# Optimization experiments

Measured on AMD Instinct MI355X. Metric: run time of the kernel, lower is better.

The kernel has to match this reference:

```python
import jax, jax.numpy as jnp
import numpy as np

N = 100000
E = 1600000
F_IN = 512
S_IN = 6
H = 64
C = 7


def gcn_conv(x, W, b, row, col, n):
    # PyG GCNConv: linear (no bias in lin), add self-loops, sym-normalize, scatter-add, + bias
    x = x @ W  # [N, out]
    loop = jnp.arange(n)
    r = jnp.concatenate([row, loop])
    c = jnp.concatenate([col, loop])
    deg = jax.ops.segment_sum(jnp.ones(r.shape, x.dtype), c, num_segments=n)
    dinv = jnp.where(deg > 0, deg ** -0.5, 0.0)
    norm = dinv[r] * dinv[c]  # [E+N]
    out = jax.ops.segment_sum(x[r] * norm[:, None], c, num_segments=n)
    return out + b


def setup_inputs() -> dict:
    key = jax.random.key(0)
    ks = jax.random.split(key, 12)
    feature = jax.random.normal(ks[0], (N, F_IN), jnp.float32)
    structure = jax.random.normal(ks[1], (N, S_IN), jnp.float32)
    edge_index = jax.random.randint(ks[2], (2, E), 0, N, dtype=jnp.int64)
    # glorot-ish param init
    def w(k, fan_in, fan_out):
        return jax.random.normal(k, (fan_in, fan_out), jnp.float32) * (1.0 / np.sqrt(fan_in))
    return {
        "feature": feature,
        "structure": structure,
        "edge_index": edge_index,
        "W_f": w(ks[3], F_IN, H), "b_f": jnp.zeros((H,), jnp.float32),
        "W_s": w(ks[4], S_IN, H), "b_s": jnp.zeros((H,), jnp.float32),
        "W_r": w(ks[5], 2 * H, C), "b_r": jnp.zeros((C,), jnp.float32),
        "emb": jax.random.normal(ks[6], (6, H), jnp.float32),
        "embW": jax.random.normal(ks[7], (H, 1), jnp.float32),
        "alpha_s": jnp.asarray(0.4, jnp.float32),
        "alpha_a": jnp.asarray(0.6, jnp.float32),
    }


def reference(feature, structure, edge_index, W_f, b_f, W_s, b_s, W_r, b_r, emb, embW, alpha_s, alpha_a):
    row, col = edge_index[0], edge_index[1]
    # branch 1: feature GCN (dropout is identity in eval mode)
    h_f = gcn_conv(feature, W_f, b_f, row, col, N)
    attr = h_f
    # embedding gate: sigmoid(emb @ embW) thresholded at 0.5 -> {0,1}
    gate = jax.nn.sigmoid(emb @ embW)  # [6,1]
    gate = jnp.where(gate < 0.5, 0.0, 1.0).astype(feature.dtype)
    struct_in = structure * gate[:, 0][None, :]  # [N,6] * [1,6]
    # branch 2: structure GCN
    h_s = gcn_conv(struct_in, W_s, b_s, row, col, N)
    struc = h_s
    # L1-normalize alphas (0.4,0.6 already sum to 1; torch does it via .data)
    denom = jax.lax.stop_gradient(jnp.abs(alpha_s) + jnp.abs(alpha_a))
    a_s = alpha_s / denom
    a_a = alpha_a / denom
    x = jnp.concatenate([attr * a_a * 2.0, struc * a_s * 2.0], axis=1)  # [N, 2H]
    y = gcn_conv(x, W_r, b_r, row, col, N)
    return (h_f, h_s, y)
```

## Files before the change

kernel.cpp:

```cpp
#include <hip/hip_runtime.h>
#include <hip/hip_bf16.h>


typedef __attribute__((ext_vector_type(8))) short bf16x8;
typedef __attribute__((ext_vector_type(4))) float f32x4;

__device__ __forceinline__ unsigned short f2bf(float x) {
    union { __hip_bfloat16 b; unsigned short u; } cv;
    cv.b = __float2bfloat16(x);
    return cv.u;
}
__device__ __forceinline__ float bf2f(unsigned short u) {
    union { unsigned u32; float f; } cv;
    cv.u32 = ((unsigned)u) << 16;
    return cv.f;
}

__device__ __forceinline__ void gload16(const void* g, void* l) {
    __builtin_amdgcn_global_load_lds(
        (const __attribute__((address_space(1))) void*)g,
        (__attribute__((address_space(3))) void*)l, 16, 0, 0);
}

__global__ __launch_bounds__(256) void setup_prep_k(const float* __restrict__ emb,
                                                    const float* __restrict__ embW,
                                                    const float* __restrict__ alpha_s,
                                                    const float* __restrict__ alpha_a,
                                                    float* __restrict__ cw,
                                                    const float* __restrict__ Wf,
                                                    unsigned short* __restrict__ WthG,
                                                    unsigned short* __restrict__ WtlG,
                                                    unsigned* __restrict__ deg, int n) {
    if (blockIdx.x == 0) {
        if (threadIdx.x >= 64) return;
        int lane = threadIdx.x;
        float w = embW[lane];
        #pragma unroll
        for (int k = 0; k < 6; k++) {
            float p = emb[k * 64 + lane] * w;
            #pragma unroll
            for (int off = 32; off; off >>= 1) p += __shfl_xor(p, off);
            if (lane == 0) cw[k] = (p < 0.0f) ? 0.0f : 1.0f;
        }
        if (lane == 0) {
            float s = alpha_s[0];
            float a = alpha_a[0];
            float inv = 1.0f / (fabsf(s) + fabsf(a));
            cw[6] = 2.0f * a * inv;
            cw[7] = 2.0f * s * inv;
        }
        return;
    }
    if (blockIdx.x <= 128) {
        int idx = (blockIdx.x - 1) * 256 + threadIdx.x;
        int k = idx >> 6, c = idx & 63;
        float w = Wf[idx];
        unsigned short h = f2bf(w);
        unsigned short l = f2bf(w - bf2f(h));
        WthG[c * 512 + k] = h;
        WtlG[c * 512 + k] = l;
        return;
    }
    int start = (blockIdx.x - 129) * 1024 + threadIdx.x;
    #pragma unroll
    for (int k = 0; k < 4; k++) {
        int w = start + k * 256;
        if (w < n) deg[w] = 0u;
    }
}

__device__ __forceinline__ bool detect32(const int* p32, int e, int E, int lane) {
    int se = (e < E) ? e : lane;
    return __any(p32[2 * se + 1] != 0);
}

#define CHUNK 4096
__global__ __launch_bounds__(256) void degfill_k(const void* __restrict__ ei,
                                                 unsigned* __restrict__ deg,
                                                 int* __restrict__ slot, int E, int n) {
    int range = blockIdx.x & 7;
    int nper = (n + 7) >> 3;
    int lo = range * nper;
    int hi = min(n, lo + nper);
    int e0 = (blockIdx.x >> 3) * CHUNK + threadIdx.x;
    int lane = threadIdx.x & 63;
    const int* p32 = (const int*)ei;
    bool is32 = detect32(p32, e0, E, lane);

    int cs[16];
    #pragma unroll
    for (int k = 0; k < 16; k++) {
        int e = e0 + k * 256;
        cs[k] = -1;
        if (e < E)
            cs[k] = is32 ? p32[E + e] : (int)((const long long*)ei)[(size_t)E + e];
    }
    #pragma unroll
    for (int k = 0; k < 16; k++) {
        int c = cs[k];
        if (c < lo || c >= hi) continue;
        int e = e0 + k * 256;
        int r = is32 ? p32[e] : (int)((const long long*)ei)[(size_t)e];
        unsigned pos = atomicAdd(&deg[c], 1u);
        if (pos < 64u) slot[((size_t)c << 6) + pos] = r;
    }
}

__global__ void dinv_ss6_k(const unsigned* __restrict__ deg, float* __restrict__ dinv,
                           const float* __restrict__ structure, const float* __restrict__ cw,
                           unsigned short* __restrict__ ss6, int n) {
    int i = blockIdx.x * 256 + threadIdx.x;
    if (i >= n) return;
    float dv = rsqrtf((float)deg[i] + 1.0f);
    dinv[i] = dv;
    #pragma unroll
    for (int k = 0; k < 6; k++) ss6[i * 8 + k] = f2bf(structure[i * 6 + k] * cw[k] * dv);
    ss6[i * 8 + 6] = 0;
    ss6[i * 8 + 7] = 0;
}

__global__ __launch_bounds__(256) void gemm_f_mfma(const float* __restrict__ feat,
                                                   const unsigned short* __restrict__ WthG,
                                                   const unsigned short* __restrict__ WtlG,
                                                   const float* __restrict__ dinv,
                                                   unsigned short* __restrict__ xs, int n) {
    __shared__ float          Afp[64 * 64];
    __shared__ unsigned short Bh[64 * 64];
    __shared__ unsigned short Bl[64 * 64];

    const int tid = threadIdx.x;
    const int w = tid >> 6, l = tid & 63;
    const int lr = l & 15, lg = l >> 4;
    const int rowbase = blockIdx.x * 64;

    f32x4 acc[4];
    #pragma unroll
    for (int nt = 0; nt < 4; nt++) acc[nt] = (f32x4)(0.0f);

    const int arow = w * 16 + lr;
    const int asw = (arow & 7) << 4;
    const char* Ab = (const char*)Afp + arow * 256;

    for (int c = 0; c < 8; c++) {
        #pragma unroll
        for (int j = 0; j < 4; j++) {
            int inst = j * 4 + w;
            int g = inst * 64 + l;
            int r = g >> 4;
            int kbs = ((g & 15) << 4) ^ ((r & 7) << 4);
            const float* src = feat + (size_t)min(rowbase + r, n - 1) * 512 + c * 64 + (kbs >> 2);
            gload16(src, (char*)Afp + inst * 1024);
        }
        #pragma unroll
        for (int j = 0; j < 2; j++) {
            int inst = j * 4 + w;
            int g = inst * 64 + l;
            int col = g >> 3;
            int kbs = ((g & 7) << 4) ^ ((col & 7) << 4);
            gload16(WthG + (size_t)col * 512 + c * 64 + (kbs >> 1), (char*)Bh + inst * 1024);
            gload16(WtlG + (size_t)col * 512 + c * 64 + (kbs >> 1), (char*)Bl + inst * 1024);
        }
        __syncthreads();
        #pragma unroll
        for (int ks = 0; ks < 2; ks++) {
            int kb0 = ks * 128 + lg * 32;
            float4 f0 = *(const float4*)(Ab + (kb0 ^ asw));
            float4 f1 = *(const float4*)(Ab + ((kb0 + 16) ^ asw));
            bf16x8 a;
            a[0] = (short)f2bf(f0.x); a[1] = (short)f2bf(f0.y);
            a[2] = (short)f2bf(f0.z); a[3] = (short)f2bf(f0.w);
            a[4] = (short)f2bf(f1.x); a[5] = (short)f2bf(f1.y);
            a[6] = (short)f2bf(f1.z); a[7] = (short)f2bf(f1.w);
            int kb = ks * 64 + lg * 16;
            #pragma unroll
            for (int nt = 0; nt < 4; nt++) {
                int bc = nt * 16 + lr;
                int cb = bc * 128 + (kb ^ ((bc & 7) << 4));
                bf16x8 bh = *(const bf16x8*)((const char*)Bh + cb);
                bf16x8 bl = *(const bf16x8*)((const char*)Bl + cb);
                acc[nt] = __builtin_amdgcn_mfma_f32_16x16x32_bf16(a, bh, acc[nt], 0, 0, 0);
                acc[nt] = __builtin_amdgcn_mfma_f32_16x16x32_bf16(a, bl, acc[nt], 0, 0, 0);
            }
        }
        __syncthreads();
    }
    int row0 = rowbase + w * 16 + lg * 4;
    #pragma unroll
    for (int reg = 0; reg < 4; reg++) {
        int gr = row0 + reg;
        if (gr < n) {
            float dv = dinv[gr];
            #pragma unroll
            for (int nt = 0; nt < 4; nt++)
                xs[(size_t)gr * 64 + nt * 16 + lr] = f2bf(acc[nt][reg] * dv);
        }
    }
}

#define GATHER8(rl, g, accv, a6v)                                              \
    {                                                                          \
        int r0 = __shfl(rl, g + 0), r1 = __shfl(rl, g + 1);                    \
        int r2 = __shfl(rl, g + 2), r3 = __shfl(rl, g + 3);                    \
        int r4 = __shfl(rl, g + 4), r5 = __shfl(rl, g + 5);                    \
        int r6 = __shfl(rl, g + 6), r7 = __shfl(rl, g + 7);                    \
        float v0 = bf2f(xs[(size_t)r0 * 64 + lane]);                           \
        float v1 = bf2f(xs[(size_t)r1 * 64 + lane]);                           \
        float v2 = bf2f(xs[(size_t)r2 * 64 + lane]);                           \
        float v3 = bf2f(xs[(size_t)r3 * 64 + lane]);                           \
        float v4 = bf2f(xs[(size_t)r4 * 64 + lane]);                           \
        float v5 = bf2f(xs[(size_t)r5 * 64 + lane]);                           \
        float v6 = bf2f(xs[(size_t)r6 * 64 + lane]);                           \
        float v7 = bf2f(xs[(size_t)r7 * 64 + lane]);                           \
        accv += ((v0 + v1) + (v2 + v3)) + ((v4 + v5) + (v6 + v7));             \
        if (lane < 6) {                                                        \
            float u0 = bf2f(ss6[r0 * 8 + lane]), u1 = bf2f(ss6[r1 * 8 + lane]);\
            float u2 = bf2f(ss6[r2 * 8 + lane]), u3 = bf2f(ss6[r3 * 8 + lane]);\
            float u4 = bf2f(ss6[r4 * 8 + lane]), u5 = bf2f(ss6[r5 * 8 + lane]);\
            float u6 = bf2f(ss6[r6 * 8 + lane]), u7 = bf2f(ss6[r7 * 8 + lane]);\
            a6v += ((u0 + u1) + (u2 + u3)) + ((u4 + u5) + (u6 + u7));          \
        }                                                                      \
    }

__global__ __launch_bounds__(256) void agg_fs_k(const unsigned short* __restrict__ xs,
                                                const unsigned short* __restrict__ ss6,
                                                const int* __restrict__ slot,
                                                const unsigned* __restrict__ deg,
                                                const float* __restrict__ dinv,
                                                const float* __restrict__ cw,
                                                const float* __restrict__ bfv,
                                                const float* __restrict__ Ws,
                                                const float* __restrict__ bs,
                                                const float* __restrict__ Wr,
                                                float* __restrict__ out_hf,
                                                float* __restrict__ out_hs,
                                                unsigned short* __restrict__ ps, int n) {
    int wid = threadIdx.x >> 6;
    int lane = threadIdx.x & 63;
    int iA = blockIdx.x * 8 + wid * 2;
    int iB = iA + 1;
    if (iA >= n) return;
    bool hasB = iB < n;

    int dA = (int)min(deg[iA], 64u);
    int dB = hasB ? (int)min(deg[iB], 64u) : 0;

    float accA = bf2f(xs[(size_t)iA * 64 + lane]);
    float accB = hasB ? bf2f(xs[(size_t)iB * 64 + lane]) : 0.0f;
    float a6A = (lane < 6) ? bf2f(ss6[iA * 8 + lane]) : 0.0f;
    float a6B = (hasB && lane < 6) ? bf2f(ss6[iB * 8 + lane]) : 0.0f;

    int rlA = (lane < dA) ? slot[((size_t)iA << 6) + lane] : 0;
    int rlB = (lane < dB) ? slot[((size_t)iB << 6) + lane] : 0;
    int gmax = max(dA, dB);
    for (int g = 0; g + 8 <= gmax; g += 8) {
        if (g + 8 <= dA) GATHER8(rlA, g, accA, a6A);
        if (g + 8 <= dB) GATHER8(rlB, g, accB, a6B);
    }
    for (int d = dA & ~7; d < dA; d++) {
        int r = __shfl(rlA, d);
        accA += bf2f(xs[(size_t)r * 64 + lane]);
        if (lane < 6) a6A += bf2f(ss6[r * 8 + lane]);
    }
    for (int d = dB & ~7; d < dB; d++) {
        int r = __shfl(rlB, d);
        accB += bf2f(xs[(size_t)r * 64 + lane]);
        if (lane < 6) a6B += bf2f(ss6[r * 8 + lane]);
    }

    #pragma unroll
    for (int node = 0; node < 2; node++) {
        if (node == 1 && !hasB) break;
        int i = node ? iB : iA;
        float acc = node ? accB : accA;
        float a6 = node ? a6B : a6A;
        float di = dinv[i];
        float hf = acc * di + bfv[lane];
        float hs = bs[lane];
        #pragma unroll
        for (int k = 0; k < 6; k++) hs += __shfl(a6, k) * di * Ws[k * 64 + lane];
        out_hf[(size_t)i * 64 + lane] = hf;
        out_hs[(size_t)i * 64 + lane] = hs;

        float fa = hf * cw[6];
        float sa = hs * cw[7];
        #pragma unroll
        for (int j = 0; j < 7; j++) {
            float v = fa * Wr[lane * 7 + j] + sa * Wr[(64 + lane) * 7 + j];
            #pragma unroll
            for (int off = 32; off; off >>= 1) v += __shfl_xor(v, off);
            if (lane == j) ps[(size_t)i * 8 + j] = f2bf(v * di);
        }
        if (lane == 7) ps[(size_t)i * 8 + 7] = 0;
    }
}

__global__ __launch_bounds__(256) void agg_y_k(const unsigned short* __restrict__ ps,
                                               const int* __restrict__ slot,
                                               const unsigned* __restrict__ deg,
                                               const float* __restrict__ dinv,
                                               const float* __restrict__ br,
                                               float* __restrict__ out_y, int n) {
    int i = blockIdx.x * 4 + (threadIdx.x >> 6);
    int lane = threadIdx.x & 63;
    if (i >= n) return;
    int es = lane >> 3, j = lane & 7;
    int cnt = (int)min(deg[i], 64u);
    const int* srow = slot + ((size_t)i << 6);
    float acc = (es == 0) ? bf2f(ps[(size_t)i * 8 + j]) : 0.0f;
    int base = 0;
    for (; base + 16 <= cnt; base += 16) {
        int ra = srow[base + es];
        int rb = srow[base + 8 + es];
        acc += bf2f(ps[(size_t)ra * 8 + j]) + bf2f(ps[(size_t)rb * 8 + j]);
    }
    for (; base < cnt; base += 8) {
        int idx = base + es;
        if (idx < cnt) acc += bf2f(ps[(size_t)srow[idx] * 8 + j]);
    }
    acc += __shfl_xor(acc, 8);
    acc += __shfl_xor(acc, 16);
    acc += __shfl_xor(acc, 32);
    if (j < 7) out_y[(size_t)i * 7 + j] = acc * dinv[i] + br[j];
}

extern "C" void kernel_launch(void* const* d_in, const int* in_sizes, int n_in,
                              void* d_out, int out_size, void* d_ws, size_t ws_size,
                              hipStream_t stream) {
    const float* feature   = (const float*)d_in[0];
    const float* structure = (const float*)d_in[1];
    const void*  ei        = d_in[2];
    const float* Wf  = (const float*)d_in[3];
    const float* bfv = (const float*)d_in[4];
    const float* Ws  = (const float*)d_in[5];
    const float* bs  = (const float*)d_in[6];
    const float* Wr  = (const float*)d_in[7];
    const float* br  = (const float*)d_in[8];
    const float* emb = (const float*)d_in[9];
    const float* embW = (const float*)d_in[10];
    const float* alpha_s = (const float*)d_in[11];
    const float* alpha_a = (const float*)d_in[12];

    const int N = in_sizes[0] / 512;
    const int E = in_sizes[2] / 2;
    const int NB = (N + 255) / 256;
    const int NZ = (N + 1023) / 1024;
    const int NCH = (E + CHUNK - 1) / CHUNK;

    float* ws = (float*)d_ws;
    size_t XS     = 0;
    size_t SS6    = XS + (size_t)N * 32;
    size_t PS     = SS6 + (size_t)N * 4;
    size_t DINV   = PS + (size_t)N * 4;
    size_t DEG    = DINV + N;
    size_t CW     = DEG + N;
    size_t WT     = CW + 16;
    size_t SLOT   = WT + 32768;

    unsigned short* xs = (unsigned short*)(ws + XS);
    unsigned short* ss6 = (unsigned short*)(ws + SS6);
    unsigned short* ps = (unsigned short*)(ws + PS);
    float* dinv = ws + DINV;
    unsigned* deg = (unsigned*)(ws + DEG);
    float* cw = ws + CW;
    unsigned short* WthG = (unsigned short*)(ws + WT);
    unsigned short* WtlG = WthG + 512 * 64;
    int* slot = (int*)(ws + SLOT);

    setup_prep_k<<<129 + NZ, 256, 0, stream>>>(emb, embW, alpha_s, alpha_a, cw,
                                               Wf, WthG, WtlG, deg, N);
    degfill_k<<<NCH * 8, 256, 0, stream>>>(ei, deg, slot, E, N);
    dinv_ss6_k<<<NB, 256, 0, stream>>>(deg, dinv, structure, cw, ss6, N);
    gemm_f_mfma<<<(N + 63) / 64, 256, 0, stream>>>(feature, WthG, WtlG, dinv, xs, N);

    float* out_hf = (float*)d_out;
    float* out_hs = out_hf + (size_t)N * 64;
    float* out_y  = out_hf + (size_t)N * 128;
    agg_fs_k<<<(N + 7) / 8, 256, 0, stream>>>(xs, ss6, slot, deg, dinv, cw,
                                              bfv, Ws, bs, Wr, out_hf, out_hs, ps, N);
    agg_y_k<<<(N + 3) / 4, 256, 0, stream>>>(ps, slot, deg, dinv, br, out_y, N);
}
```

Measured before the change: 264.9 us.

## Fuse degree fill with feature GEMM and apply source normalization in aggregation

Merges the edge bucketing/degree-count kernel and the feature GEMM into one launch with interleaved block roles, so the atomic-heavy scatter and the MFMA GEMM run concurrently instead of back to back. This removes the dependence of the GEMM on dinv: xs and ss6 are stored unnormalized, and the per-source dinv is recomputed from deg inside the gather loops. The dinv_ss6 kernel and dinv buffer are dropped, with the structure gating folded into the setup kernel. In exchange, each gathered neighbour costs an extra deg load and rsqrt, and the mixed block roles may share compute units less evenly.

Result: no change. 264.2 us (-0.2%).

```diff
diff --git a/kernel.cpp b/kernel.cpp
--- a/kernel.cpp
+++ b/kernel.cpp
@@ -30,7 +30,9 @@
                                                     const float* __restrict__ Wf,
                                                     unsigned short* __restrict__ WthG,
                                                     unsigned short* __restrict__ WtlG,
-                                                    unsigned* __restrict__ deg, int n) {
+                                                    unsigned* __restrict__ deg,
+                                                    const float* __restrict__ structure,
+                                                    unsigned short* __restrict__ ss6, int n) {
     if (blockIdx.x == 0) {
         if (threadIdx.x >= 64) return;
         int lane = threadIdx.x;
@@ -61,11 +63,28 @@
         WtlG[c * 512 + k] = l;
         return;
     }
+    int lane = threadIdx.x & 63;
+    float wv = embW[lane];
+    float g[6];
+    #pragma unroll
+    for (int k = 0; k < 6; k++) {
+        float p = emb[k * 64 + lane] * wv;
+        #pragma unroll
+        for (int off = 32; off; off >>= 1) p += __shfl_xor(p, off);
+        g[k] = (p < 0.0f) ? 0.0f : 1.0f;
+    }
     int start = (blockIdx.x - 129) * 1024 + threadIdx.x;
     #pragma unroll
-    for (int k = 0; k < 4; k++) {
-        int w = start + k * 256;
-        if (w < n) deg[w] = 0u;
+    for (int j = 0; j < 4; j++) {
+        int i = start + j * 256;
+        if (i < n) {
+            deg[i] = 0u;
+            #pragma unroll
+            for (int k = 0; k < 6; k++)
+                ss6[i * 8 + k] = f2bf(structure[i * 6 + k] * g[k]);
+            ss6[i * 8 + 6] = 0;
+            ss6[i * 8 + 7] = 0;
+        }
     }
 }
 
@@ -75,63 +94,58 @@
 }
 
 #define CHUNK 4096
-__global__ __launch_bounds__(256) void degfill_k(const void* __restrict__ ei,
-                                                 unsigned* __restrict__ deg,
-                                                 int* __restrict__ slot, int E, int n) {
-    int range = blockIdx.x & 7;
-    int nper = (n + 7) >> 3;
-    int lo = range * nper;
-    int hi = min(n, lo + nper);
-    int e0 = (blockIdx.x >> 3) * CHUNK + threadIdx.x;
-    int lane = threadIdx.x & 63;
-    const int* p32 = (const int*)ei;
-    bool is32 = detect32(p32, e0, E, lane);
-
-    int cs[16];
-    #pragma unroll
-    for (int k = 0; k < 16; k++) {
-        int e = e0 + k * 256;
-        cs[k] = -1;
-        if (e < E)
-            cs[k] = is32 ? p32[E + e] : (int)((const long long*)ei)[(size_t)E + e];
-    }
-    #pragma unroll
-    for (int k = 0; k < 16; k++) {
-        int c = cs[k];
-        if (c < lo || c >= hi) continue;
-        int e = e0 + k * 256;
-        int r = is32 ? p32[e] : (int)((const long long*)ei)[(size_t)e];
-        unsigned pos = atomicAdd(&deg[c], 1u);
-        if (pos < 64u) slot[((size_t)c << 6) + pos] = r;
-    }
-}
-
-__global__ void dinv_ss6_k(const unsigned* __restrict__ deg, float* __restrict__ dinv,
-                           const float* __restrict__ structure, const float* __restrict__ cw,
-                           unsigned short* __restrict__ ss6, int n) {
-    int i = blockIdx.x * 256 + threadIdx.x;
-    if (i >= n) return;
-    float dv = rsqrtf((float)deg[i] + 1.0f);
-    dinv[i] = dv;
-    #pragma unroll
-    for (int k = 0; k < 6; k++) ss6[i * 8 + k] = f2bf(structure[i * 6 + k] * cw[k] * dv);
-    ss6[i * 8 + 6] = 0;
-    ss6[i * 8 + 7] = 0;
-}
-
-__global__ __launch_bounds__(256) void gemm_f_mfma(const float* __restrict__ feat,
-                                                   const unsigned short* __restrict__ WthG,
-                                                   const unsigned short* __restrict__ WtlG,
-                                                   const float* __restrict__ dinv,
-                                                   unsigned short* __restrict__ xs, int n) {
+
+__global__ __launch_bounds__(256) void fused_k(const void* __restrict__ ei,
+                                               unsigned* __restrict__ deg,
+                                               int* __restrict__ slot, int E, int n,
+                                               int GB,
+                                               const float* __restrict__ feat,
+                                               const unsigned short* __restrict__ WthG,
+                                               const unsigned short* __restrict__ WtlG,
+                                               unsigned short* __restrict__ xs) {
     __shared__ float          Afp[64 * 64];
     __shared__ unsigned short Bh[64 * 64];
     __shared__ unsigned short Bl[64 * 64];
 
+    const int b = blockIdx.x;
     const int tid = threadIdx.x;
+    const bool is_gemm = (b % 3 == 2) && (b / 3 < GB);
+
+    if (!is_gemm) {
+        int eb = b - min(GB, b / 3);
+        int range = eb & 7;
+        int nper = (n + 7) >> 3;
+        int lo = range * nper;
+        int hi = min(n, lo + nper);
+        int e0 = (eb >> 3) * CHUNK + tid;
+        int lane = tid & 63;
+        const int* p32 = (const int*)ei;
+        bool is32 = detect32(p32, e0, E, lane);
+
+        int cs[16];
+        #pragma unroll
+        for (int k = 0; k < 16; k++) {
+            int e = e0 + k * 256;
+            cs[k] = -1;
+            if (e < E)
+                cs[k] = is32 ? p32[E + e] : (int)((const long long*)ei)[(size_t)E + e];
+        }
+        #pragma unroll
+        for (int k = 0; k < 16; k++) {
+            int c = cs[k];
+            if (c < lo || c >= hi) continue;
+            int e = e0 + k * 256;
+            int r = is32 ? p32[e] : (int)((const long long*)ei)[(size_t)e];
+            unsigned pos = atomicAdd(&deg[c], 1u);
+            if (pos < 64u) slot[((size_t)c << 6) + pos] = r;
+        }
+        return;
+    }
+
+    const int gb = b / 3;
     const int w = tid >> 6, l = tid & 63;
     const int lr = l & 15, lg = l >> 4;
-    const int rowbase = blockIdx.x * 64;
+    const int rowbase = gb * 64;
 
     f32x4 acc[4];
     #pragma unroll
@@ -189,13 +203,14 @@
     for (int reg = 0; reg < 4; reg++) {
         int gr = row0 + reg;
         if (gr < n) {
-            float dv = dinv[gr];
             #pragma unroll
             for (int nt = 0; nt < 4; nt++)
-                xs[(size_t)gr * 64 + nt * 16 + lr] = f2bf(acc[nt][reg] * dv);
-        }
-    }
-}
+                xs[(size_t)gr * 64 + nt * 16 + lr] = f2bf(acc[nt][reg]);
+        }
+    }
+}
+
+__device__ __forceinline__ float dnv(unsigned d) { return rsqrtf((float)d + 1.0f); }
 
 #define GATHER8(rl, g, accv, a6v)                                              \
     {                                                                          \
@@ -203,20 +218,28 @@
         int r2 = __shfl(rl, g + 2), r3 = __shfl(rl, g + 3);                    \
         int r4 = __shfl(rl, g + 4), r5 = __shfl(rl, g + 5);                    \
         int r6 = __shfl(rl, g + 6), r7 = __shfl(rl, g + 7);                    \
-        float v0 = bf2f(xs[(size_t)r0 * 64 + lane]);                           \
-        float v1 = bf2f(xs[(size_t)r1 * 64 + lane]);                           \
-        float v2 = bf2f(xs[(size_t)r2 * 64 + lane]);                           \
-        float v3 = bf2f(xs[(size_t)r3 * 64 + lane]);                           \
-        float v4 = bf2f(xs[(size_t)r4 * 64 + lane]);                           \
-        float v5 = bf2f(xs[(size_t)r5 * 64 + lane]);                           \
-        float v6 = bf2f(xs[(size_t)r6 * 64 + lane]);                           \
-        float v7 = bf2f(xs[(size_t)r7 * 64 + lane]);                           \
+        float q0 = dnv(deg[r0]), q1 = dnv(deg[r1]);                            \
+        float q2 = dnv(deg[r2]), q3 = dnv(deg[r3]);                            \
+        float q4 = dnv(deg[r4]), q5 = dnv(deg[r5]);                            \
+        float q6 = dnv(deg[r6]), q7 = dnv(deg[r7]);                            \
+        float v0 = bf2f(xs[(size_t)r0 * 64 + lane]) * q0;                      \
+        float v1 = bf2f(xs[(size_t)r1 * 64 + lane]) * q1;                      \
+        float v2 = bf2f(xs[(size_t)r2 * 64 + lane]) * q2;                      \
+        float v3 = bf2f(xs[(size_t)r3 * 64 + lane]) * q3;                      \
+        float v4 = bf2f(xs[(size_t)r4 * 64 + lane]) * q4;                      \
+        float v5 = bf2f(xs[(size_t)r5 * 64 + lane]) * q5;                      \
+        float v6 = bf2f(xs[(size_t)r6 * 64 + lane]) * q6;                      \
+        float v7 = bf2f(xs[(size_t)r7 * 64 + lane]) * q7;                      \
         accv += ((v0 + v1) + (v2 + v3)) + ((v4 + v5) + (v6 + v7));             \
         if (lane < 6) {                                                        \
-            float u0 = bf2f(ss6[r0 * 8 + lane]), u1 = bf2f(ss6[r1 * 8 + lane]);\
-            float u2 = bf2f(ss6[r2 * 8 + lane]), u3 = bf2f(ss6[r3 * 8 + lane]);\
-            float u4 = bf2f(ss6[r4 * 8 + lane]), u5 = bf2f(ss6[r5 * 8 + lane]);\
-            float u6 = bf2f(ss6[r6 * 8 + lane]), u7 = bf2f(ss6[r7 * 8 + lane]);\
+            float u0 = bf2f(ss6[r0 * 8 + lane]) * q0;                          \
+            float u1 = bf2f(ss6[r1 * 8 + lane]) * q1;                          \
+            float u2 = bf2f(ss6[r2 * 8 + lane]) * q2;                          \
+            float u3 = bf2f(ss6[r3 * 8 + lane]) * q3;                          \
+            float u4 = bf2f(ss6[r4 * 8 + lane]) * q4;                          \
+            float u5 = bf2f(ss6[r5 * 8 + lane]) * q5;                          \
+            float u6 = bf2f(ss6[r6 * 8 + lane]) * q6;                          \
+            float u7 = bf2f(ss6[r7 * 8 + lane]) * q7;                          \
             a6v += ((u0 + u1) + (u2 + u3)) + ((u4 + u5) + (u6 + u7));          \
         }                                                                      \
     }
@@ -225,7 +248,6 @@
                                                 const unsigned short* __restrict__ ss6,
                                                 const int* __restrict__ slot,
                                                 const unsigned* __restrict__ deg,
-                                                const float* __restrict__ dinv,
                                                 const float* __restrict__ cw,
                                                 const float* __restrict__ bfv,
                                                 const float* __restrict__ Ws,
@@ -241,13 +263,17 @@
     if (iA >= n) return;
     bool hasB = iB < n;
 
-    int dA = (int)min(deg[iA], 64u);
-    int dB = hasB ? (int)min(deg[iB], 64u) : 0;
-
-    float accA = bf2f(xs[(size_t)iA * 64 + lane]);
-    float accB = hasB ? bf2f(xs[(size_t)iB * 64 + lane]) : 0.0f;
-    float a6A = (lane < 6) ? bf2f(ss6[iA * 8 + lane]) : 0.0f;
-    float a6B = (hasB && lane < 6) ? bf2f(ss6[iB * 8 + lane]) : 0.0f;
+    unsigned dgA = deg[iA];
+    unsigned dgB = hasB ? deg[iB] : 0u;
+    float dviA = dnv(dgA);
+    float dviB = dnv(dgB);
+    int dA = (int)min(dgA, 64u);
+    int dB = hasB ? (int)min(dgB, 64u) : 0;
+
+    float accA = bf2f(xs[(size_t)iA * 64 + lane]) * dviA;
+    float accB = hasB ? bf2f(xs[(size_t)iB * 64 + lane]) * dviB : 0.0f;
+    float a6A = (lane < 6) ? bf2f(ss6[iA * 8 + lane]) * dviA : 0.0f;
+    float a6B = (hasB && lane < 6) ? bf2f(ss6[iB * 8 + lane]) * dviB : 0.0f;
 
     int rlA = (lane < dA) ? slot[((size_t)iA << 6) + lane] : 0;
     int rlB = (lane < dB) ? slot[((size_t)iB << 6) + lane] : 0;
@@ -258,13 +284,15 @@
     }
     for (int d = dA & ~7; d < dA; d++) {
         int r = __shfl(rlA, d);
-        accA += bf2f(xs[(size_t)r * 64 + lane]);
-        if (lane < 6) a6A += bf2f(ss6[r * 8 + lane]);
+        float q = dnv(deg[r]);
+        accA += bf2f(xs[(size_t)r * 64 + lane]) * q;
+        if (lane < 6) a6A += bf2f(ss6[r * 8 + lane]) * q;
     }
     for (int d = dB & ~7; d < dB; d++) {
         int r = __shfl(rlB, d);
-        accB += bf2f(xs[(size_t)r * 64 + lane]);
-        if (lane < 6) a6B += bf2f(ss6[r * 8 + lane]);
+        float q = dnv(deg[r]);
+        accB += bf2f(xs[(size_t)r * 64 + lane]) * q;
+        if (lane < 6) a6B += bf2f(ss6[r * 8 + lane]) * q;
     }
 
     #pragma unroll
@@ -273,7 +301,7 @@
         int i = node ? iB : iA;
         float acc = node ? accB : accA;
         float a6 = node ? a6B : a6A;
-        float di = dinv[i];
+        float di = node ? dviB : dviA;
         float hf = acc * di + bfv[lane];
         float hs = bs[lane];
         #pragma unroll
@@ -297,7 +325,6 @@
 __global__ __launch_bounds__(256) void agg_y_k(const unsigned short* __restrict__ ps,
                                                const int* __restrict__ slot,
                                                const unsigned* __restrict__ deg,
-                                               const float* __restrict__ dinv,
                                                const float* __restrict__ br,
                                                float* __restrict__ out_y, int n) {
     int i = blockIdx.x * 4 + (threadIdx.x >> 6);
@@ -320,7 +347,7 @@
     acc += __shfl_xor(acc, 8);
     acc += __shfl_xor(acc, 16);
     acc += __shfl_xor(acc, 32);
-    if (j < 7) out_y[(size_t)i * 7 + j] = acc * dinv[i] + br[j];
+    if (j < 7) out_y[(size_t)i * 7 + j] = acc * dnv(deg[i]) + br[j];
 }
 
 extern "C" void kernel_launch(void* const* d_in, const int* in_sizes, int n_in,
@@ -342,16 +369,16 @@
 
     const int N = in_sizes[0] / 512;
     const int E = in_sizes[2] / 2;
-    const int NB = (N + 255) / 256;
     const int NZ = (N + 1023) / 1024;
     const int NCH = (E + CHUNK - 1) / CHUNK;
+    const int EB = NCH * 8;
+    const int GB = (N + 63) / 64;
 
     float* ws = (float*)d_ws;
     size_t XS     = 0;
     size_t SS6    = XS + (size_t)N * 32;
     size_t PS     = SS6 + (size_t)N * 4;
-    size_t DINV   = PS + (size_t)N * 4;
-    size_t DEG    = DINV + N;
+    size_t DEG    = PS + (size_t)N * 4;
     size_t CW     = DEG + N;
     size_t WT     = CW + 16;
     size_t SLOT   = WT + 32768;
@@ -359,7 +386,6 @@
     unsigned short* xs = (unsigned short*)(ws + XS);
     unsigned short* ss6 = (unsigned short*)(ws + SS6);
     unsigned short* ps = (unsigned short*)(ws + PS);
-    float* dinv = ws + DINV;
     unsigned* deg = (unsigned*)(ws + DEG);
     float* cw = ws + CW;
     unsigned short* WthG = (unsigned short*)(ws + WT);
@@ -367,15 +393,14 @@
     int* slot = (int*)(ws + SLOT);
 
     setup_prep_k<<<129 + NZ, 256, 0, stream>>>(emb, embW, alpha_s, alpha_a, cw,
-                                               Wf, WthG, WtlG, deg, N);
-    degfill_k<<<NCH * 8, 256, 0, stream>>>(ei, deg, slot, E, N);
-    dinv_ss6_k<<<NB, 256, 0, stream>>>(deg, dinv, structure, cw, ss6, N);
-    gemm_f_mfma<<<(N + 63) / 64, 256, 0, stream>>>(feature, WthG, WtlG, dinv, xs, N);
+                                               Wf, WthG, WtlG, deg, structure, ss6, N);
+    fused_k<<<EB + GB, 256, 0, stream>>>(ei, deg, slot, E, N, GB,
+                                         feature, WthG, WtlG, xs);
 
     float* out_hf = (float*)d_out;
     float* out_hs = out_hf + (size_t)N * 64;
     float* out_y  = out_hf + (size_t)N * 128;
-    agg_fs_k<<<(N + 7) / 8, 256, 0, stream>>>(xs, ss6, slot, deg, dinv, cw,
+    agg_fs_k<<<(N + 7) / 8, 256, 0, stream>>>(xs, ss6, slot, deg, cw,
                                               bfv, Ws, bs, Wr, out_hf, out_hs, ps, N);
-    agg_y_k<<<(N + 3) / 4, 256, 0, stream>>>(ps, slot, deg, dinv, br, out_y, N);
-}
+    agg_y_k<<<(N + 3) / 4, 256, 0, stream>>>(ps, slot, deg, br, out_y, N);
+}
```

## Co-schedule degree fill with feature GEMM in one launch, defer dinv scaling

Applied to the files above, without the earlier changes.

Merges the edge-scatter degree/slot fill kernel and the feature GEMM into one kernel whose blocks interleave the two roles, so the latency-bound atomic scatter and the compute-bound MFMA GEMM overlap on the device. Because the GEMM no longer waits for degrees, the dinv scaling moves to a new post pass that rescales xs and ss6 once degrees are known. The gated structure product moves into the setup kernel. The cost is an extra read and write of xs plus a second bf16 rounding step, which may slightly change accuracy.

Result: no change. 265.4 us (+0.2%).

```diff
diff --git a/kernel.cpp b/kernel.cpp
--- a/kernel.cpp
+++ b/kernel.cpp
@@ -15,6 +15,7 @@
     cv.u32 = ((unsigned)u) << 16;
     return cv.f;
 }
+__device__ __forceinline__ float dnv(unsigned d) { return rsqrtf((float)d + 1.0f); }
 
 __device__ __forceinline__ void gload16(const void* g, void* l) {
     __builtin_amdgcn_global_load_lds(
@@ -30,7 +31,9 @@
                                                     const float* __restrict__ Wf,
                                                     unsigned short* __restrict__ WthG,
                                                     unsigned short* __restrict__ WtlG,
-                                                    unsigned* __restrict__ deg, int n) {
+                                                    unsigned* __restrict__ deg,
+                                                    const float* __restrict__ structure,
+                                                    unsigned short* __restrict__ ss6, int n) {
     if (blockIdx.x == 0) {
         if (threadIdx.x >= 64) return;
         int lane = threadIdx.x;
@@ -61,11 +64,28 @@
         WtlG[c * 512 + k] = l;
         return;
     }
+    int lane = threadIdx.x & 63;
+    float wv = embW[lane];
+    float g[6];
+    #pragma unroll
+    for (int k = 0; k < 6; k++) {
+        float p = emb[k * 64 + lane] * wv;
+        #pragma unroll
+        for (int off = 32; off; off >>= 1) p += __shfl_xor(p, off);
+        g[k] = (p < 0.0f) ? 0.0f : 1.0f;
+    }
     int start = (blockIdx.x - 129) * 1024 + threadIdx.x;
     #pragma unroll
-    for (int k = 0; k < 4; k++) {
-        int w = start + k * 256;
-        if (w < n) deg[w] = 0u;
+    for (int j = 0; j < 4; j++) {
+        int i = start + j * 256;
+        if (i < n) {
+            deg[i] = 0u;
+            #pragma unroll
+            for (int k = 0; k < 6; k++)
+                ss6[i * 8 + k] = f2bf(structure[i * 6 + k] * g[k]);
+            ss6[i * 8 + 6] = 0;
+            ss6[i * 8 + 7] = 0;
+        }
     }
 }
 
@@ -75,63 +95,58 @@
 }
 
 #define CHUNK 4096
-__global__ __launch_bounds__(256) void degfill_k(const void* __restrict__ ei,
-                                                 unsigned* __restrict__ deg,
-                                                 int* __restrict__ slot, int E, int n) {
-    int range = blockIdx.x & 7;
-    int nper = (n + 7) >> 3;
-    int lo = range * nper;
-    int hi = min(n, lo + nper);
-    int e0 = (blockIdx.x >> 3) * CHUNK + threadIdx.x;
-    int lane = threadIdx.x & 63;
-    const int* p32 = (const int*)ei;
-    bool is32 = detect32(p32, e0, E, lane);
-
-    int cs[16];
-    #pragma unroll
-    for (int k = 0; k < 16; k++) {
-        int e = e0 + k * 256;
-        cs[k] = -1;
-        if (e < E)
-            cs[k] = is32 ? p32[E + e] : (int)((const long long*)ei)[(size_t)E + e];
-    }
-    #pragma unroll
-    for (int k = 0; k < 16; k++) {
-        int c = cs[k];
-        if (c < lo || c >= hi) continue;
-        int e = e0 + k * 256;
-        int r = is32 ? p32[e] : (int)((const long long*)ei)[(size_t)e];
-        unsigned pos = atomicAdd(&deg[c], 1u);
-        if (pos < 64u) slot[((size_t)c << 6) + pos] = r;
-    }
-}
-
-__global__ void dinv_ss6_k(const unsigned* __restrict__ deg, float* __restrict__ dinv,
-                           const float* __restrict__ structure, const float* __restrict__ cw,
-                           unsigned short* __restrict__ ss6, int n) {
-    int i = blockIdx.x * 256 + threadIdx.x;
-    if (i >= n) return;
-    float dv = rsqrtf((float)deg[i] + 1.0f);
-    dinv[i] = dv;
-    #pragma unroll
-    for (int k = 0; k < 6; k++) ss6[i * 8 + k] = f2bf(structure[i * 6 + k] * cw[k] * dv);
-    ss6[i * 8 + 6] = 0;
-    ss6[i * 8 + 7] = 0;
-}
-
-__global__ __launch_bounds__(256) void gemm_f_mfma(const float* __restrict__ feat,
-                                                   const unsigned short* __restrict__ WthG,
-                                                   const unsigned short* __restrict__ WtlG,
-                                                   const float* __restrict__ dinv,
-                                                   unsigned short* __restrict__ xs, int n) {
+
+__global__ __launch_bounds__(256) void fused_k(const void* __restrict__ ei,
+                                               unsigned* __restrict__ deg,
+                                               int* __restrict__ slot, int E, int n,
+                                               int GB,
+                                               const float* __restrict__ feat,
+                                               const unsigned short* __restrict__ WthG,
+                                               const unsigned short* __restrict__ WtlG,
+                                               unsigned short* __restrict__ xs) {
     __shared__ float          Afp[64 * 64];
     __shared__ unsigned short Bh[64 * 64];
     __shared__ unsigned short Bl[64 * 64];
 
+    const int b = blockIdx.x;
     const int tid = threadIdx.x;
+    const bool is_gemm = (b % 3 == 2) && (b / 3 < GB);
+
+    if (!is_gemm) {
+        int eb = b - min(GB, b / 3);
+        int range = eb & 7;
+        int nper = (n + 7) >> 3;
+        int lo = range * nper;
+        int hi = min(n, lo + nper);
+        int e0 = (eb >> 3) * CHUNK + tid;
+        int lane = tid & 63;
+        const int* p32 = (const int*)ei;
+        bool is32 = detect32(p32, e0, E, lane);
+
+        int cs[16];
+        #pragma unroll
+        for (int k = 0; k < 16; k++) {
+            int e = e0 + k * 256;
+            cs[k] = -1;
+            if (e < E)
+                cs[k] = is32 ? p32[E + e] : (int)((const long long*)ei)[(size_t)E + e];
+        }
+        #pragma unroll
+        for (int k = 0; k < 16; k++) {
+            int c = cs[k];
+            if (c < lo || c >= hi) continue;
+            int e = e0 + k * 256;
+            int r = is32 ? p32[e] : (int)((const long long*)ei)[(size_t)e];
+            unsigned pos = atomicAdd(&deg[c], 1u);
+            if (pos < 64u) slot[((size_t)c << 6) + pos] = r;
+        }
+        return;
+    }
+
+    const int gb = b / 3;
     const int w = tid >> 6, l = tid & 63;
     const int lr = l & 15, lg = l >> 4;
-    const int rowbase = blockIdx.x * 64;
+    const int rowbase = gb * 64;
 
     f32x4 acc[4];
     #pragma unroll
@@ -189,12 +204,25 @@
     for (int reg = 0; reg < 4; reg++) {
         int gr = row0 + reg;
         if (gr < n) {
-            float dv = dinv[gr];
             #pragma unroll
             for (int nt = 0; nt < 4; nt++)
-                xs[(size_t)gr * 64 + nt * 16 + lr] = f2bf(acc[nt][reg] * dv);
-        }
-    }
+                xs[(size_t)gr * 64 + nt * 16 + lr] = f2bf(acc[nt][reg]);
+        }
+    }
+}
+
+__global__ __launch_bounds__(256) void post_k(const unsigned* __restrict__ deg,
+                                              float* __restrict__ dinv,
+                                              unsigned short* __restrict__ xs,
+                                              unsigned short* __restrict__ ss6, int n) {
+    int i = blockIdx.x * 4 + (threadIdx.x >> 6);
+    int lane = threadIdx.x & 63;
+    if (i >= n) return;
+    float dv = dnv(deg[i]);
+    if (lane == 0) dinv[i] = dv;
+    size_t o = (size_t)i * 64 + lane;
+    xs[o] = f2bf(bf2f(xs[o]) * dv);
+    if (lane < 6) ss6[i * 8 + lane] = f2bf(bf2f(ss6[i * 8 + lane]) * dv);
 }
 
 #define GATHER8(rl, g, accv, a6v)                                              \
@@ -342,9 +370,10 @@
 
     const int N = in_sizes[0] / 512;
     const int E = in_sizes[2] / 2;
-    const int NB = (N + 255) / 256;
     const int NZ = (N + 1023) / 1024;
     const int NCH = (E + CHUNK - 1) / CHUNK;
+    const int EB = NCH * 8;
+    const int GB = (N + 63) / 64;
 
     float* ws = (float*)d_ws;
     size_t XS     = 0;
@@ -367,10 +396,10 @@
     int* slot = (int*)(ws + SLOT);
 
     setup_prep_k<<<129 + NZ, 256, 0, stream>>>(emb, embW, alpha_s, alpha_a, cw,
-                                               Wf, WthG, WtlG, deg, N);
-    degfill_k<<<NCH * 8, 256, 0, stream>>>(ei, deg, slot, E, N);
-    dinv_ss6_k<<<NB, 256, 0, stream>>>(deg, dinv, structure, cw, ss6, N);
-    gemm_f_mfma<<<(N + 63) / 64, 256, 0, stream>>>(feature, WthG, WtlG, dinv, xs, N);
+                                               Wf, WthG, WtlG, deg, structure, ss6, N);
+    fused_k<<<EB + GB, 256, 0, stream>>>(ei, deg, slot, E, N, GB,
+                                         feature, WthG, WtlG, xs);
+    post_k<<<(N + 3) / 4, 256, 0, stream>>>(deg, dinv, xs, ss6, N);
 
     float* out_hf = (float*)d_out;
     float* out_hs = out_hf + (size_t)N * 64;
```
